# Kernel optimization log

Measured on AMD Instinct MI355X. Metric: run time of the kernel, lower is better.

Reference implementation:

```python
import jax, jax.numpy as jnp
import numpy as np

IN_FEATS = 128
OUT_FEATS = 128
ASSIGN_DIM = 256
BATCH_SIZE = 8
N = 12288
E = 196608
CPG = ASSIGN_DIM // BATCH_SIZE  # clusters per graph (block width of the mask)


def setup_inputs() -> dict:
    key = jax.random.key(0)
    ks = jax.random.split(key, 6)
    x = jax.random.normal(ks[0], (N, IN_FEATS), dtype=jnp.float32)
    edge_index = jax.random.randint(ks[1], (2, E), 0, N, dtype=jnp.int32)
    batch = jnp.sort(jax.random.randint(ks[2], (N,), 0, BATCH_SIZE, dtype=jnp.int32))
    s = 1.0 / np.sqrt(2 * IN_FEATS)
    W_embd = jax.random.uniform(ks[3], (2 * IN_FEATS, OUT_FEATS), minval=-s, maxval=s, dtype=jnp.float32)
    b_embd = jnp.zeros((OUT_FEATS,), jnp.float32)
    W_pool = jax.random.uniform(ks[4], (2 * IN_FEATS, ASSIGN_DIM), minval=-s, maxval=s, dtype=jnp.float32)
    b_pool = jnp.zeros((ASSIGN_DIM,), jnp.float32)
    return dict(x=x, edge_index=edge_index, batch=batch,
                W_embd=W_embd, b_embd=b_embd, W_pool=W_pool, b_pool=b_pool)


def _sage_conv(x, src, dst, W, b):
    # GraphSAGE mean aggregator, concat([self, agg]) @ W + b, row L2-normalize.
    agg = jax.ops.segment_sum(x[src], dst, num_segments=N)                 # [N, F]
    deg = jax.ops.segment_sum(jnp.ones((E,), x.dtype), dst, num_segments=N)
    agg = agg / jnp.maximum(deg, 1.0)[:, None]
    h = jnp.concatenate([x, agg], axis=-1) @ W + b
    return h / jnp.maximum(jnp.linalg.norm(h, axis=-1, keepdims=True), 1e-12)


def _masked_softmax_nonme(m, mask):
    # memory_efficient=False branch of masked_softmax
    r = jax.nn.softmax(m * mask, axis=-1)
    r = r * mask
    return r / (r.sum(axis=-1, keepdims=True) + 1e-13)


def reference(x, edge_index, batch, W_embd, b_embd, W_pool, b_pool):
    src, dst = edge_index[0], edge_index[1]
    embed = _sage_conv(x, src, dst, W_embd, b_embd)    # [N, out_feats]
    pooled = _sage_conv(x, src, dst, W_pool, b_pool)   # [N, assign_dim]

    # block-diagonal mask: node i sees the assign columns of its own graph
    col_graph = jnp.arange(ASSIGN_DIM, dtype=batch.dtype) // CPG
    mask = (batch[:, None] == col_graph[None, :]).astype(pooled.dtype)  # [N, assign_dim]

    result = _masked_softmax_nonme(pooled, mask)        # [N, assign_dim]
    h = result.T @ embed                                # [assign_dim, out_feats]

    # adjacency coarsening: S^T A S with edge weights = 1 (duplicates sum)
    Ar = jax.ops.segment_sum(result[dst], src, num_segments=N)  # A @ result
    adj_new = result.T @ Ar                              # [assign_dim, assign_dim]

    # link prediction loss: ||A_dense - S S^T||_F / N^2 (dense NxN, as original)
    A_dense = jnp.zeros((N, N), result.dtype).at[src, dst].add(1.0)
    adj_loss = jnp.linalg.norm(A_dense - result @ result.T) / (N ** 2)

    # entropy loss over Categorical(probs=mask): uniform over each block
    p = mask / mask.sum(axis=-1, keepdims=True)
    ent = -jnp.sum(jnp.where(p > 0, p * jnp.log(jnp.where(p > 0, p, 1.0)), 0.0), axis=-1)
    entropy_loss = ent.sum()

    return adj_new, h, adj_loss, entropy_loss
```

## Files before the change

kernel.cpp:

```cpp
#include <hip/hip_runtime.h>
#include <math.h>

#define NN 12288
#define EE 196608
#define FIN 128
#define AD 256
#define NG 8
#define ACH 32
#define GCH 16
#define BCAP 128
#define APITCH 8256
#define HPITCH 4160
#define GPITCH 1088

using short8 = __attribute__((ext_vector_type(8))) short;
using floatx4 = __attribute__((ext_vector_type(4))) float;

__device__ __forceinline__ unsigned short f2bf(float f) {
  union { float f; unsigned u; } v; v.f = f;
  unsigned r = v.u + 0x7FFFu + ((v.u >> 16) & 1u);
  return (unsigned short)(r >> 16);
}


__global__ __launch_bounds__(256) void k_setup(const float* __restrict__ We, const float* __restrict__ be,
    const float* __restrict__ Wp, const float* __restrict__ bp, const int* __restrict__ batch,
    unsigned* cnt_dst, unsigned* cnt_src, double* acc, unsigned* done,
    unsigned short* __restrict__ WTb, float* __restrict__ bcat, int* __restrict__ gstart) {
  unsigned i = blockIdx.x * 256u + threadIdx.x;
  if (i < 384u * 256u) {
    unsigned n = i >> 8, k = i & 255u;
    float v = (n < 128u) ? We[k * 128u + n] : Wp[k * 256u + (n - 128u)];
    WTb[i] = f2bf(v);
  }
  if (i < 384u) bcat[i] = (i < 128u) ? be[i] : bp[i - 128u];
  if (i < NN) { cnt_dst[i] = 0u; cnt_src[i] = 0u; }
  if (i < 3u) acc[i] = 0.0;
  if (i == 3u) *done = 0u;
  if (i <= NG) {
    int g = (int)i, lo = 0, hi = NN;
    while (lo < hi) { int mid = (lo + hi) >> 1; if (batch[mid] < g) lo = mid + 1; else hi = mid; }
    gstart[g] = lo;
  }
}


__global__ __launch_bounds__(256) void k_edgeB(const int* __restrict__ src, const int* __restrict__ dst,
    const int* __restrict__ batch,
    unsigned* cnt_dst, unsigned* cnt_src, int* __restrict__ bdst, int* __restrict__ bsrc) {
  unsigned e = blockIdx.x * 256u + threadIdx.x;
  if (e >= EE) return;
  int s = src[e], d = dst[e];
  unsigned p = atomicAdd(&cnt_dst[d], 1u);
  if (p < BCAP) bdst[(size_t)d * BCAP + p] = s;
  int gd = batch[d];
  unsigned q = atomicAdd(&cnt_src[s], 1u);
  if (q < BCAP) bsrc[(size_t)s * BCAP + q] = (gd << 14) | d;
}


__global__ __launch_bounds__(256) void k_dupagg(const float* __restrict__ x,
    const unsigned* __restrict__ cnt_dst, const int* __restrict__ bdst,
    unsigned short* __restrict__ Zb, unsigned* __restrict__ dup_part) {
  int node = blockIdx.x * 4 + (threadIdx.x >> 6);
  int lane = threadIdx.x & 63;
  unsigned deg = cnt_dst[node];
  unsigned m = deg < BCAP ? deg : BCAP;
  const int* bk = bdst + (size_t)node * BCAP;
  const float2* x2 = (const float2*)x;
  unsigned cnt = 0;
  float ax = 0.f, ay = 0.f;
  int si = ((unsigned)lane < m) ? bk[lane] : -2;
  for (unsigned j = 0; j < m; j++) {
    int sj = bk[j];
    cnt += (si == sj) ? 1u : 0u;
    float2 v = x2[(size_t)sj * 64 + lane];
    ax += v.x; ay += v.y;
  }
  for (unsigned i0 = 64; i0 < m; i0 += 64) {
    int si2 = (i0 + lane < m) ? bk[i0 + lane] : -2;
    for (unsigned j = 0; j < m; j++) cnt += (si2 == bk[j]) ? 1u : 0u;
  }
#pragma unroll
  for (int o = 32; o >= 1; o >>= 1) cnt += __shfl_xor(cnt, o, 64);
  if (lane == 0) dup_part[node] = cnt;
  float inv = 1.f / fmaxf((float)deg, 1.f);
  float2 sv = x2[(size_t)node * 64 + lane];
  ushort2* Zb2 = (ushort2*)Zb;
  ushort2 a; a.x = f2bf(sv.x); a.y = f2bf(sv.y);
  ushort2 mm; mm.x = f2bf(ax * inv); mm.y = f2bf(ay * inv);
  Zb2[(size_t)node * 128 + lane] = a;
  Zb2[(size_t)node * 128 + 64 + lane] = mm;
}


__global__ __launch_bounds__(256) void k_gemmnorm(const unsigned short* __restrict__ Zb,
    const unsigned short* __restrict__ WTb, const float* __restrict__ bcat,
    const int* __restrict__ batch, float* __restrict__ embed, float* __restrict__ Rc) {
  __shared__ unsigned short Bl[24 * 512];
  __shared__ unsigned short Al[4 * 512];
  int t = threadIdx.x;
  int gm = blockIdx.x * 64;
  int w = t >> 6, l = t & 63;

  floatx4 acc[24] = {};

  for (int kc = 0; kc < 8; kc++) {
    __syncthreads();
#pragma unroll
    for (int i = 0; i < 7; i++) {
      int p = t + i * 256;
      if (p < 1536) {
        int n = p >> 2, quad = p & 3;
        uint4 v = *(const uint4*)&WTb[(size_t)n * 256 + kc * 32 + quad * 8];
        *(uint4*)&Bl[(n >> 4) * 512 + ((n & 15) + 16 * quad) * 8] = v;
      } else {
        int p2 = p - 1536;
        int m = p2 >> 2, quad = p2 & 3;
        uint4 v = *(const uint4*)&Zb[(size_t)(gm + m) * 256 + kc * 32 + quad * 8];
        *(uint4*)&Al[(m >> 4) * 512 + ((m & 15) + 16 * quad) * 8] = v;
      }
    }
    __syncthreads();
    short8 a = *(const short8*)&Al[w * 512 + l * 8];
#pragma unroll
    for (int tt = 0; tt < 24; tt++) {
      short8 b = *(const short8*)&Bl[tt * 512 + l * 8];
      acc[tt] = __builtin_amdgcn_mfma_f32_16x16x32_bf16(a, b, acc[tt], 0, 0, 0);
    }
  }

  int col16 = l & 15, quad = l >> 4;
#pragma unroll
  for (int tt = 0; tt < 24; tt++) {
    float b = bcat[tt * 16 + col16];
    acc[tt][0] += b; acc[tt][1] += b; acc[tt][2] += b; acc[tt][3] += b;
  }

#pragma unroll
  for (int r = 0; r < 4; r++) {
    int node = gm + w * 16 + quad * 4 + r;
    float ss = 0.f;
#pragma unroll
    for (int tt = 0; tt < 8; tt++) { float v = acc[tt][r]; ss += v * v; }
#pragma unroll
    for (int o = 8; o >= 1; o >>= 1) ss += __shfl_xor(ss, o, 64);
    float inv = 1.f / fmaxf(sqrtf(ss), 1e-12f);
#pragma unroll
    for (int tt = 0; tt < 8; tt++)
      embed[(size_t)node * 128 + tt * 16 + col16] = acc[tt][r] * inv;
    float ss2 = 0.f;
#pragma unroll
    for (int tt = 8; tt < 24; tt++) { float v = acc[tt][r]; ss2 += v * v; }
#pragma unroll
    for (int o = 8; o >= 1; o >>= 1) ss2 += __shfl_xor(ss2, o, 64);
    float inv2 = 1.f / fmaxf(sqrtf(ss2), 1e-12f);
    int g = batch[node];
    float v0 = 0.f, v1 = 0.f;
#pragma unroll
    for (int tg = 0; tg < 8; tg++) {
      bool sel = (tg == g);
      v0 = sel ? acc[8 + 2 * tg][r] : v0;
      v1 = sel ? acc[9 + 2 * tg][r] : v1;
    }
    v0 *= inv2; v1 *= inv2;
    float mx = fmaxf(v0, v1);
#pragma unroll
    for (int o = 8; o >= 1; o >>= 1) mx = fmaxf(mx, __shfl_xor(mx, o, 64));
    float e0 = expf(v0 - mx), e1 = expf(v1 - mx);
    float sm = e0 + e1;
#pragma unroll
    for (int o = 8; o >= 1; o >>= 1) sm += __shfl_xor(sm, o, 64);
    float rr = 1.f / sm;
    Rc[(size_t)node * 32 + col16] = e0 * rr;
    Rc[(size_t)node * 32 + 16 + col16] = e1 * rr;
  }
}


__global__ __launch_bounds__(256) void k_ar(const float* __restrict__ Rc,
    const unsigned* __restrict__ cnt_src, const int* __restrict__ bsrc,
    float* __restrict__ Ar) {
  int node = blockIdx.x * 4 + (threadIdx.x >> 6);
  int lane = threadIdx.x & 63;
  int lg = lane >> 3, li = lane & 7;
  unsigned deg = cnt_src[node];
  unsigned m = deg < BCAP ? deg : BCAP;
  const int* bk = bsrc + (size_t)node * BCAP;
  float4 acc = {0.f, 0.f, 0.f, 0.f};
  const float4* R4 = (const float4*)Rc;
  for (unsigned k = 0; k < m; k++) {
    int packed = bk[k];
    int d = packed & 16383, g = packed >> 14;
    if (lg == g) {
      float4 r = R4[(size_t)d * 8 + li];
      acc.x += r.x; acc.y += r.y; acc.z += r.z; acc.w += r.w;
    }
  }
  ((float4*)Ar)[(size_t)node * 64 + lane] = acc;
}


__global__ __launch_bounds__(256) void k_big3(const float* __restrict__ Rc,
    const float* __restrict__ embed, const float* __restrict__ Ar, const int* __restrict__ gstart,
    float* __restrict__ part_h, float* __restrict__ part_adj, float* __restrict__ Gpart) {
  int role = blockIdx.z;
  int g = blockIdx.x, ch = blockIdx.y;
  if (role == 2 && ch >= GCH) return;
  int s0 = gstart[g], e0 = gstart[g + 1];
  int nch = (role == 2) ? GCH : ACH;
  int per = (e0 - s0 + nch - 1) / nch;
  int i0 = s0 + ch * per;
  int i1 = i0 + per; if (i1 > e0) i1 = e0;
  int t = threadIdx.x;
  __shared__ float rcs[128][32];

  if (role == 0) {
    int f4 = t & 31, c1g = t >> 5;
    float4 acc[4] = {};
    const float4* E4 = (const float4*)embed;
    for (int ib = i0; ib < i1; ib += 64) {
      int cnt = i1 - ib; if (cnt > 64) cnt = 64;
      __syncthreads();
      const float4* s4 = (const float4*)(Rc + (size_t)ib * 32);
      for (int idx = t; idx < cnt * 8; idx += 256) ((float4*)rcs)[idx] = s4[idx];
      __syncthreads();
      for (int n = 0; n < cnt; n++) {
        float4 e4 = E4[(size_t)(ib + n) * 32 + f4];
        float4 r = *(const float4*)&rcs[n][c1g * 4];
        float rv[4] = {r.x, r.y, r.z, r.w};
#pragma unroll
        for (int j = 0; j < 4; j++) {
          acc[j].x += rv[j] * e4.x; acc[j].y += rv[j] * e4.y;
          acc[j].z += rv[j] * e4.z; acc[j].w += rv[j] * e4.w;
        }
      }
    }
    float* p = part_h + (size_t)(g * ACH + ch) * HPITCH;
#pragma unroll
    for (int j = 0; j < 4; j++)
      *(float4*)&p[(c1g * 4 + j) * 128 + f4 * 4] = acc[j];
  } else if (role == 1) {
    int c2q = t & 63, c1g = t >> 6;
    float4 acc[8] = {};
    const float4* Ar4 = (const float4*)Ar;
    for (int ib = i0; ib < i1; ib += 64) {
      int cnt = i1 - ib; if (cnt > 64) cnt = 64;
      __syncthreads();
      const float4* s4 = (const float4*)(Rc + (size_t)ib * 32);
      for (int idx = t; idx < cnt * 8; idx += 256) ((float4*)rcs)[idx] = s4[idx];
      __syncthreads();
      for (int n = 0; n < cnt; n++) {
        float4 a4 = Ar4[(size_t)(ib + n) * 64 + c2q];
        float4 r0 = *(const float4*)&rcs[n][c1g * 8];
        float4 r1 = *(const float4*)&rcs[n][c1g * 8 + 4];
        float rv[8] = {r0.x, r0.y, r0.z, r0.w, r1.x, r1.y, r1.z, r1.w};
#pragma unroll
        for (int j = 0; j < 8; j++) {
          acc[j].x += rv[j] * a4.x; acc[j].y += rv[j] * a4.y;
          acc[j].z += rv[j] * a4.z; acc[j].w += rv[j] * a4.w;
        }
      }
    }
    float* p = part_adj + (size_t)(g * ACH + ch) * APITCH;
#pragma unroll
    for (int j = 0; j < 8; j++)
      *(float4*)&p[(c1g * 8 + j) * 256 + c2q * 4] = acc[j];
  } else {
    int c2q = t & 7, c1 = t >> 3;
    float4 acc = {};
    for (int ib = i0; ib < i1; ib += 128) {
      int cnt = i1 - ib; if (cnt > 128) cnt = 128;
      __syncthreads();
      const float4* s4 = (const float4*)(Rc + (size_t)ib * 32);
      for (int idx = t; idx < cnt * 8; idx += 256) ((float4*)rcs)[idx] = s4[idx];
      __syncthreads();
      for (int n = 0; n < cnt; n++) {
        float4 r2 = *(const float4*)&rcs[n][c2q * 4];
        float r1 = rcs[n][c1];
        acc.x += r1 * r2.x; acc.y += r1 * r2.y; acc.z += r1 * r2.z; acc.w += r1 * r2.w;
      }
    }
    *(float4*)&Gpart[(size_t)(g * GCH + ch) * GPITCH + c1 * 32 + c2q * 4] = acc;
  }
}


__global__ __launch_bounds__(256) void k_red3(const float* __restrict__ part_adj,
    const float* __restrict__ part_h, const float* __restrict__ Gpart,
    const unsigned* __restrict__ dup_part,
    float* __restrict__ outa, float* __restrict__ outh,
    double* __restrict__ acc, unsigned* __restrict__ done, float* __restrict__ out) {
  int b = blockIdx.x, t = threadIdx.x;
  int lane = t & 63;
  if (b < 256) {
    int i = b * 256 + t;
    int g = i >> 13, off = i & 8191;
    const float* base = part_adj + (size_t)g * ACH * APITCH + off;
    float s = 0.f;
#pragma unroll
    for (int ch = 0; ch < ACH; ch++) s += base[(size_t)ch * APITCH];
    outa[i] = s;
    if (t == b) atomicAdd(&acc[0], (double)s);
  } else if (b < 384) {
    int j = (b - 256) * 256 + t;
    int g = j >> 12, off = j & 4095;
    const float* base = part_h + (size_t)g * ACH * HPITCH + off;
    float s = 0.f;
#pragma unroll
    for (int ch = 0; ch < ACH; ch++) s += base[(size_t)ch * HPITCH];
    outh[j] = s;
  } else if (b < 416) {
    int j = (b - 384) * 256 + t;
    int g = j >> 10, off = j & 1023;
    const float* base = Gpart + (size_t)g * GCH * GPITCH + off;
    float s = 0.f;
#pragma unroll
    for (int ch = 0; ch < GCH; ch++) s += base[(size_t)ch * GPITCH];
    double g2 = (double)s * (double)s;
#pragma unroll
    for (int o = 32; o >= 1; o >>= 1) g2 += __shfl_xor(g2, o, 64);
    if (lane == 0) atomicAdd(&acc[1], g2);
  } else {
    int j = (b - 416) * 256 + t;
    double a2 = (double)dup_part[j];
#pragma unroll
    for (int o = 32; o >= 1; o >>= 1) a2 += __shfl_xor(a2, o, 64);
    if (lane == 0) atomicAdd(&acc[2], a2);
  }
  __syncthreads();
  if (t == 0) {
    unsigned prev = atomicAdd(done, 1u);
    if (prev == gridDim.x - 1) {
      double trf = atomicAdd(&acc[0], 0.0);
      double g2f = atomicAdd(&acc[1], 0.0);
      double a2f = atomicAdd(&acc[2], 0.0);
      double val = a2f - 2.0 * trf + g2f;
      if (val < 0.0) val = 0.0;
      out[98304] = (float)(sqrt(val) / ((double)NN * (double)NN));
      out[98305] = (float)((double)NN * log(32.0));
    }
  }
}


extern "C" void kernel_launch(void* const* d_in, const int* in_sizes, int n_in,
                              void* d_out, int out_size, void* d_ws, size_t ws_size,
                              hipStream_t stream) {
  const float* x = (const float*)d_in[0];
  const int* ei = (const int*)d_in[1];
  const int* src = ei;
  const int* dst = ei + EE;
  const int* batch = (const int*)d_in[2];
  const float* Wemb = (const float*)d_in[3];
  const float* bemb = (const float*)d_in[4];
  const float* Wpool = (const float*)d_in[5];
  const float* bpool = (const float*)d_in[6];
  float* out = (float*)d_out;

  char* w = (char*)d_ws;
  size_t off = 0;
  auto A = [&](size_t bytes) -> char* {
    char* p = w + off;
    off += (bytes + 255) & ~(size_t)255;
    return p;
  };
  unsigned* cnt_dst = (unsigned*)A(NN * 4);
  unsigned* cnt_src = (unsigned*)A(NN * 4);
  int* bdst = (int*)A((size_t)NN * BCAP * 4);
  int* bsrc = (int*)A((size_t)NN * BCAP * 4);
  int* gstart = (int*)A(64);
  unsigned* dup_part = (unsigned*)A(NN * 4);
  double* acc = (double*)A(3 * 8);
  unsigned* done = (unsigned*)A(4);
  unsigned short* Zb = (unsigned short*)A((size_t)NN * 256 * 2);
  float* embed = (float*)A((size_t)NN * FIN * 4);
  float* Rc = (float*)A((size_t)NN * 32 * 4);
  float* Ar = (float*)A((size_t)NN * AD * 4);
  unsigned short* WTb = (unsigned short*)A(384 * 256 * 2);
  float* bcat = (float*)A(384 * 4);
  float* part_h = (float*)A((size_t)8 * ACH * HPITCH * 4);
  float* part_adj = (float*)A((size_t)8 * ACH * APITCH * 4);
  float* Gpart = (float*)A((size_t)8 * GCH * GPITCH * 4);
  (void)ws_size; (void)in_sizes; (void)n_in; (void)out_size;

  k_setup<<<dim3(384), dim3(256), 0, stream>>>(Wemb, bemb, Wpool, bpool, batch,
      cnt_dst, cnt_src, acc, done, WTb, bcat, gstart);
  k_edgeB<<<dim3(EE / 256), dim3(256), 0, stream>>>(src, dst, batch, cnt_dst, cnt_src, bdst, bsrc);
  k_dupagg<<<dim3(NN / 4), dim3(256), 0, stream>>>(x, cnt_dst, bdst, Zb, dup_part);
  k_gemmnorm<<<dim3(NN / 64), dim3(256), 0, stream>>>(Zb, WTb, bcat, batch, embed, Rc);
  k_ar<<<dim3(NN / 4), dim3(256), 0, stream>>>(Rc, cnt_src, bsrc, Ar);
  k_big3<<<dim3(8, ACH, 3), dim3(256), 0, stream>>>(Rc, embed, Ar, gstart, part_h, part_adj, Gpart);
  k_red3<<<dim3(464), dim3(256), 0, stream>>>(part_adj, part_h, Gpart, dup_part,
      out, out + 65536, acc, done, out);
}
```

Measured before the change: 191.0 us.

## Split edge loops across wave halves and lane groups with shuffled neighbor indices

In k_dupagg, neighbor indices are now broadcast with wave shuffles instead of repeated global reads. Feature gathers use float4 loads, and the two half-waves each take alternate edges before a cross-half reduction. In k_ar, the 8 lane groups each handle a different edge per iteration and scatter into 8 per-graph accumulators that are reduced with shuffles. Previously every edge was a serial load that only one lane group used. The aim is more parallel memory requests and fewer redundant index loads, at the cost of more registers and shuffle-reduction work.

```diff
diff --git a/kernel.cpp b/kernel.cpp
--- a/kernel.cpp
+++ b/kernel.cpp
@@ -64,33 +64,60 @@
     unsigned short* __restrict__ Zb, unsigned* __restrict__ dup_part) {
   int node = blockIdx.x * 4 + (threadIdx.x >> 6);
   int lane = threadIdx.x & 63;
+  int h = lane >> 5, c = lane & 31;
   unsigned deg = cnt_dst[node];
   unsigned m = deg < BCAP ? deg : BCAP;
+  unsigned m64 = m < 64u ? m : 64u;
   const int* bk = bdst + (size_t)node * BCAP;
-  const float2* x2 = (const float2*)x;
+  const float4* x4 = (const float4*)x;
+
+  int si = ((unsigned)lane < m) ? bk[lane] : -2;
+
   unsigned cnt = 0;
-  float ax = 0.f, ay = 0.f;
-  int si = ((unsigned)lane < m) ? bk[lane] : -2;
-  for (unsigned j = 0; j < m; j++) {
-    int sj = bk[j];
+  for (unsigned j = 0; j < m64; j++) {
+    int sj = __shfl(si, (int)j, 64);
     cnt += (si == sj) ? 1u : 0u;
-    float2 v = x2[(size_t)sj * 64 + lane];
-    ax += v.x; ay += v.y;
-  }
-  for (unsigned i0 = 64; i0 < m; i0 += 64) {
-    int si2 = (i0 + lane < m) ? bk[i0 + lane] : -2;
-    for (unsigned j = 0; j < m; j++) cnt += (si2 == bk[j]) ? 1u : 0u;
-  }
+  }
+
+  float4 a = {0.f, 0.f, 0.f, 0.f};
+  for (unsigned e = (unsigned)h; e < m64; e += 2) {
+    int sj = __shfl(si, (int)e, 64);
+    float4 v = x4[(size_t)sj * 32 + c];
+    a.x += v.x; a.y += v.y; a.z += v.z; a.w += v.w;
+  }
+
+  if (m > 64u) {
+    for (unsigned e = 64u + (unsigned)h; e < m; e += 2) {
+      int sj = bk[e];
+      float4 v = x4[(size_t)sj * 32 + c];
+      a.x += v.x; a.y += v.y; a.z += v.z; a.w += v.w;
+    }
+    for (unsigned j = 64; j < m; j++) cnt += (si == bk[j]) ? 1u : 0u;
+    for (unsigned i0 = 64; i0 < m; i0 += 64) {
+      int si2 = (i0 + lane < m) ? bk[i0 + lane] : -3;
+      for (unsigned j = 0; j < m; j++) cnt += (si2 == bk[j]) ? 1u : 0u;
+    }
+  }
+
+  a.x += __shfl_xor(a.x, 32, 64);
+  a.y += __shfl_xor(a.y, 32, 64);
+  a.z += __shfl_xor(a.z, 32, 64);
+  a.w += __shfl_xor(a.w, 32, 64);
+
 #pragma unroll
   for (int o = 32; o >= 1; o >>= 1) cnt += __shfl_xor(cnt, o, 64);
   if (lane == 0) dup_part[node] = cnt;
+
   float inv = 1.f / fmaxf((float)deg, 1.f);
-  float2 sv = x2[(size_t)node * 64 + lane];
-  ushort2* Zb2 = (ushort2*)Zb;
-  ushort2 a; a.x = f2bf(sv.x); a.y = f2bf(sv.y);
-  ushort2 mm; mm.x = f2bf(ax * inv); mm.y = f2bf(ay * inv);
-  Zb2[(size_t)node * 128 + lane] = a;
-  Zb2[(size_t)node * 128 + 64 + lane] = mm;
+  float4 sv = x4[(size_t)node * 32 + c];
+  ushort4 o4;
+  if (h == 0) {
+    o4.x = f2bf(sv.x); o4.y = f2bf(sv.y); o4.z = f2bf(sv.z); o4.w = f2bf(sv.w);
+  } else {
+    o4.x = f2bf(a.x * inv); o4.y = f2bf(a.y * inv);
+    o4.z = f2bf(a.z * inv); o4.w = f2bf(a.w * inv);
+  }
+  ((ushort4*)Zb)[(size_t)node * 64 + h * 32 + c] = o4;
 }
 
 
@@ -186,18 +213,58 @@
   int lg = lane >> 3, li = lane & 7;
   unsigned deg = cnt_src[node];
   unsigned m = deg < BCAP ? deg : BCAP;
+  unsigned m64 = m < 64u ? m : 64u;
   const int* bk = bsrc + (size_t)node * BCAP;
-  float4 acc = {0.f, 0.f, 0.f, 0.f};
   const float4* R4 = (const float4*)Rc;
-  for (unsigned k = 0; k < m; k++) {
-    int packed = bk[k];
+
+  int pk = ((unsigned)lane < m) ? bk[lane] : (8 << 14);
+
+  float4 acc[8] = {};
+  for (unsigned k = 0; k < m64; k += 8) {
+    int packed = __shfl(pk, (int)(k + (unsigned)lg), 64);
     int d = packed & 16383, g = packed >> 14;
-    if (lg == g) {
+    float4 r = R4[(size_t)d * 8 + li];
+#pragma unroll
+    for (int j = 0; j < 8; j++) {
+      float wj = (g == j) ? 1.f : 0.f;
+      acc[j].x = fmaf(wj, r.x, acc[j].x);
+      acc[j].y = fmaf(wj, r.y, acc[j].y);
+      acc[j].z = fmaf(wj, r.z, acc[j].z);
+      acc[j].w = fmaf(wj, r.w, acc[j].w);
+    }
+  }
+
+  if (m > 64u) {
+    for (unsigned e2 = 64; e2 < m; e2++) {
+      int packed = bk[e2];
+      int d = packed & 16383, g = packed >> 14;
       float4 r = R4[(size_t)d * 8 + li];
-      acc.x += r.x; acc.y += r.y; acc.z += r.z; acc.w += r.w;
-    }
-  }
-  ((float4*)Ar)[(size_t)node * 64 + lane] = acc;
+      bool mine = (lg == g);
+#pragma unroll
+      for (int j = 0; j < 8; j++) {
+        float wj = (mine && g == j) ? 1.f : 0.f;
+        acc[j].x = fmaf(wj, r.x, acc[j].x);
+        acc[j].y = fmaf(wj, r.y, acc[j].y);
+        acc[j].z = fmaf(wj, r.z, acc[j].z);
+        acc[j].w = fmaf(wj, r.w, acc[j].w);
+      }
+    }
+  }
+
+#pragma unroll
+  for (int j = 0; j < 8; j++) {
+#pragma unroll
+    for (int o = 8; o <= 32; o <<= 1) {
+      acc[j].x += __shfl_xor(acc[j].x, o, 64);
+      acc[j].y += __shfl_xor(acc[j].y, o, 64);
+      acc[j].z += __shfl_xor(acc[j].z, o, 64);
+      acc[j].w += __shfl_xor(acc[j].w, o, 64);
+    }
+  }
+  float4 wv = acc[0];
+#pragma unroll
+  for (int j = 1; j < 8; j++) if (lg == j) wv = acc[j];
+  ((float4*)Ar)[(size_t)node * 64 + lane] = wv;
 }
 
 
```

New measurement: 174.1 us. 8.8% less time.
